# Performance work log

Measured on AMD Instinct MI355X. Metric: run time of the kernel, lower is better.

The kernel has to match this reference:

```python
import jax, jax.numpy as jnp
import numpy as np

B, H, W, C = 4, 48, 48, 768
L = H * W
D_STATE, D_CONV, D_INNER = 16, 4, C  # expand=1
DT_RANK = (C + 15) // 16  # 48


def generate_cross_scan_indices(Hh, Ww):
    indices = []
    visited = set()
    ch, cw = Hh // 2, Ww // 2
    indices.append((ch, cw)); visited.add((ch, cw))
    for radius in range(1, max(Hh, Ww)):
        for r in range(1, radius + 1):
            p = (ch - r, cw)
            if 0 <= p[0] < Hh and 0 <= p[1] < Ww and p not in visited: indices.append(p); visited.add(p)
        for r in range(1, radius + 1):
            p = (ch, cw + r)
            if 0 <= p[0] < Hh and 0 <= p[1] < Ww and p not in visited: indices.append(p); visited.add(p)
        for r in range(1, radius + 1):
            p = (ch + r, cw)
            if 0 <= p[0] < Hh and 0 <= p[1] < Ww and p not in visited: indices.append(p); visited.add(p)
        for r in range(1, radius + 1):
            p = (ch, cw - r)
            if 0 <= p[0] < Hh and 0 <= p[1] < Ww and p not in visited: indices.append(p); visited.add(p)
        for r in range(1, radius + 1):
            for p in [(ch - r, cw + r), (ch + r, cw + r), (ch + r, cw - r), (ch - r, cw - r)]:
                if 0 <= p[0] < Hh and 0 <= p[1] < Ww and p not in visited: indices.append(p); visited.add(p)
        for i in range(-radius, radius + 1):
            for j in range(-radius, radius + 1):
                p = (ch + i, cw + j)
                if 0 <= p[0] < Hh and 0 <= p[1] < Ww and p not in visited: indices.append(p); visited.add(p)
    return np.array([i * Ww + j for i, j in indices], dtype=np.int32)


def _mamba_params(key, scale=0.02):
    ks = jax.random.split(key, 6)
    return dict(
        in_w=jax.random.normal(ks[0], (2 * D_INNER, C)) * scale,
        conv_w=jax.random.normal(ks[1], (D_INNER, 1, D_CONV)) * scale,
        conv_b=jnp.zeros((D_INNER,)),
        xproj_w=jax.random.normal(ks[2], (DT_RANK + 2 * D_STATE, D_INNER)) * scale,
        dt_w=jax.random.normal(ks[3], (D_INNER, DT_RANK)) * scale,
        dt_b=jax.random.normal(ks[4], (D_INNER,)) * 0.1,
        A_log=jnp.broadcast_to(jnp.log(jnp.arange(1, D_STATE + 1, dtype=jnp.float32)), (D_INNER, D_STATE)).copy(),
        Dp=jnp.ones((D_INNER,)),
        out_w=jax.random.normal(ks[5], (C, D_INNER)) * scale,
    )


def setup_inputs() -> dict:
    key = jax.random.key(0)
    kx, kf, kb, k1, k2 = jax.random.split(key, 5)
    fp = _mamba_params(kf)
    bp = _mamba_params(kb)
    inp = {
        'x': jax.random.normal(kx, (B, L, C), dtype=jnp.float32),
        'scan_idx': jnp.asarray(generate_cross_scan_indices(H, W)),
        'norm_g': jnp.ones((C,)), 'norm_b': jnp.zeros((C,)),
        'fuse_w1': jax.random.normal(k1, (C, 2 * C)) * 0.02, 'fuse_b1': jnp.zeros((C,)),
        'fuse_w2': jax.random.normal(k2, (C, C)) * 0.02, 'fuse_b2': jnp.zeros((C,)),
    }
    for pre, p in (('f_', fp), ('b_', bp)):
        for n, v in p.items():
            inp[pre + n] = v
    return inp


def silu(v):
    return v * jax.nn.sigmoid(v)


def mamba(x, in_w, conv_w, conv_b, xproj_w, dt_w, dt_b, A_log, Dp, out_w):
    Bn, Ln, _ = x.shape
    xz = x @ in_w.T                      # [B,L,2*d_inner]
    xi, z = jnp.split(xz, 2, axis=-1)
    # causal depthwise conv1d, kernel D_CONV, left pad D_CONV-1
    xp = jnp.pad(xi, ((0, 0), (D_CONV - 1, 0), (0, 0)))
    xc = sum(conv_w[:, 0, k] * xp[:, k:k + Ln, :] for k in range(D_CONV)) + conv_b
    xc = silu(xc)                        # [B,L,d_inner]
    x_dbl = xc @ xproj_w.T
    dt, Bm, Cm = jnp.split(x_dbl, [DT_RANK, DT_RANK + D_STATE], axis=-1)
    dt = jax.nn.softplus(dt @ dt_w.T + dt_b)  # [B,L,d_inner]
    A = -jnp.exp(A_log)                  # [d_inner,d_state]

    def step(h, inps):
        dt_t, B_t, C_t, x_t = inps       # [B,d],[B,s],[B,s],[B,d]
        dA = jnp.exp(dt_t[:, :, None] * A)
        h = dA * h + (dt_t * x_t)[:, :, None] * B_t[:, None, :]
        y = jnp.einsum('bds,bs->bd', h, C_t)
        return h, y

    h0 = jnp.zeros((Bn, D_INNER, D_STATE), xc.dtype)
    xs = (dt.transpose(1, 0, 2), Bm.transpose(1, 0, 2), Cm.transpose(1, 0, 2), xc.transpose(1, 0, 2))
    _, ys = jax.lax.scan(step, h0, xs)
    y = ys.transpose(1, 0, 2) + Dp * xc
    y = y * silu(z)
    return y @ out_w.T


def reference(x, scan_idx, norm_g, norm_b, fuse_w1, fuse_b1, fuse_w2, fuse_b2,
              f_in_w, f_conv_w, f_conv_b, f_xproj_w, f_dt_w, f_dt_b, f_A_log, f_Dp, f_out_w,
              b_in_w, b_conv_w, b_conv_b, b_xproj_w, b_dt_w, b_dt_b, b_A_log, b_Dp, b_out_w):
    residual = x
    mu = x.mean(-1, keepdims=True)
    var = ((x - mu) ** 2).mean(-1, keepdims=True)
    xn = (x - mu) / jnp.sqrt(var + 1e-6) * norm_g + norm_b
    rev = jnp.argsort(scan_idx)
    xf = mamba(xn[:, scan_idx, :], f_in_w, f_conv_w, f_conv_b, f_xproj_w, f_dt_w, f_dt_b, f_A_log, f_Dp, f_out_w)[:, rev, :]
    flip = scan_idx[::-1]
    xb = mamba(xn[:, flip, :], b_in_w, b_conv_w, b_conv_b, b_xproj_w, b_dt_w, b_dt_b, b_A_log, b_Dp, b_out_w)[:, jnp.argsort(flip), :]
    fused = jnp.concatenate([xf, xb], axis=-1)
    h = jax.nn.gelu(fused @ fuse_w1.T + fuse_b1, approximate=False)
    out = h @ fuse_w2.T + fuse_b2
    return out + residual
```

## Files before the change

### kernel.cpp

```cpp
#include <hip/hip_runtime.h>
#include <hip/hip_bf16.h>
#include <cmath>

#define BB 4
#define LL 2304
#define CC 768
#define DSTATE 16
#define DINNER 768
#define DTRANK 48
#define MTOK (BB*LL)
#define NCH 48
#define LCH (LL/NCH)

#define S_XZ   14155776L
#define S_XC   7077888L
#define S_DT   7077888L
#define S_BC   294912L
#define S_YB   7077888L
#define S_AP   2359296L
#define S_XCR  79036416L

#define L2E 1.4426950408889634f

typedef __bf16 bf16_t;
typedef __bf16 bf16x8 __attribute__((ext_vector_type(8)));
typedef float  f32x4  __attribute__((ext_vector_type(4)));

__device__ __forceinline__ float silu_f(float v){ return v / (1.0f + __expf(-v)); }
__device__ __forceinline__ float softplus_f(float v){
    return fmaxf(v,0.f) + __logf(1.0f + __expf(-fabsf(v)));
}

typedef __attribute__((address_space(3))) void  lds_vt;
typedef __attribute__((address_space(1))) void  gbl_vt;
__device__ __forceinline__ void async_copy16(const void* g, void* l){
    __builtin_amdgcn_global_load_lds((const gbl_vt*)g, (lds_vt*)l, 16, 0, 0);
}


__global__ __launch_bounds__(256)
void wconv_k(const float* __restrict__ a0, const float* __restrict__ a1,
             const float* __restrict__ a2, const float* __restrict__ a3,
             const float* __restrict__ a4, const float* __restrict__ a5,
             bf16_t* __restrict__ dst)
{
    const int cum[7]  = {0,1179648,2359296,3538944,4128768,4153344,4177920};
    const int dofs[6] = {0,1179648,2359296,3538944,4718592,5332992};
    const float* srcs[6] = {a0,a1,a2,a3,a4,a5};
    int idx = blockIdx.x*256 + threadIdx.x;
    if (idx >= 4177920) return;
    int seg = 0;
    while (idx >= cum[seg+1]) ++seg;
    dst[dofs[seg] + idx - cum[seg]] = (bf16_t)srcs[seg][idx - cum[seg]];
}

__global__ __launch_bounds__(256)
void transp_k(const float* __restrict__ s0, const float* __restrict__ s1,
              bf16_t* __restrict__ d0, bf16_t* __restrict__ d1)
{
    __shared__ float tile[32][33];
    const float* src = blockIdx.z ? s1 : s0;
    bf16_t* dst = blockIdx.z ? d1 : d0;
    int c0 = blockIdx.y*32, d0c = blockIdx.x*32;
    int tx = threadIdx.x & 31, ty = threadIdx.x >> 5;
#pragma unroll
    for (int r=0;r<4;++r)
        tile[ty+8*r][tx] = src[(long)(c0+ty+8*r)*768 + d0c+tx];
    __syncthreads();
#pragma unroll
    for (int r=0;r<4;++r)
        dst[(long)(d0c+ty+8*r)*768 + c0+tx] = (bf16_t)tile[tx][ty+8*r];
}

__global__ __launch_bounds__(256)
void inv_k(const int* __restrict__ sidx, int* __restrict__ rf, int* __restrict__ rb)
{
    int t = blockIdx.x*256 + threadIdx.x;
    if (t >= LL) return;
    rf[sidx[t]] = t;
    rb[sidx[LL-1-t]] = t;
}

__global__ __launch_bounds__(256)
void combo_k(const float* __restrict__ dtw, const float* __restrict__ xproj,
             bf16_t* __restrict__ dst)
{
    __shared__ float row[48];
    int n = blockIdx.x;
    if (threadIdx.x < 48) row[threadIdx.x] = dtw[n*48 + threadIdx.x];
    __syncthreads();
#pragma unroll
    for (int kk=0; kk<3; ++kk){
        int k = threadIdx.x + 256*kk;
        float s = 0.f;
#pragma unroll 8
        for (int r=0; r<48; ++r) s += row[r]*xproj[r*768 + k];
        dst[n*768 + k] = (bf16_t)s;
    }
}

__global__ __launch_bounds__(256)
void ln_k(const float* __restrict__ x, const float* __restrict__ g,
          const float* __restrict__ bta, bf16_t* __restrict__ xn)
{
    int row = blockIdx.x;
    const float* xr = x + (long)row*CC;
    int tid = threadIdx.x;
    float v[3];
#pragma unroll
    for (int r=0;r<3;++r) v[r] = xr[tid + 256*r];
    float s  = v[0]+v[1]+v[2];
    float s2 = v[0]*v[0]+v[1]*v[1]+v[2]*v[2];
    __shared__ float red[8];
    for (int o=32;o;o>>=1){ s += __shfl_down(s,o); s2 += __shfl_down(s2,o); }
    int wv = tid>>6, ln = tid&63;
    if (ln==0){ red[wv]=s; red[4+wv]=s2; }
    __syncthreads();
    if (tid==0){
        red[0] = red[0]+red[1]+red[2]+red[3];
        red[4] = red[4]+red[5]+red[6]+red[7];
    }
    __syncthreads();
    float mu  = red[0]*(1.0f/CC);
    float var = red[4]*(1.0f/CC) - mu*mu;
    float rstd = rsqrtf(var + 1e-6f);
#pragma unroll
    for (int r=0;r<3;++r){
        int c = tid + 256*r;
        xn[(long)row*CC + c] = (bf16_t)((v[r]-mu)*rstd*g[c] + bta[c]);
    }
}

__global__ __launch_bounds__(256)
void conv_k(const bf16_t* __restrict__ xzT, const float* __restrict__ cw0,
            const float* __restrict__ cw1, const float* __restrict__ cb0,
            const float* __restrict__ cb1, bf16_t* __restrict__ xcT,
            bf16_t* __restrict__ xcR0, bf16_t* __restrict__ xcR1)
{
    const int dir = blockIdx.y;
    const bf16_t* src = xzT + (long)dir*S_XZ;
    bf16_t* dstT = xcT + (long)dir*S_XC;
    bf16_t* dstR = dir ? xcR1 : xcR0;
    const float* cw = dir ? cw1 : cw0;
    const float* cb = dir ? cb1 : cb0;
    int idx = blockIdx.x*256 + threadIdx.x;
    int d = idx % 768;
    int chunk = idx / 768;
    int tb = chunk*2;
    int r0 = chunk*16;

    bf16x8 c0 = *(const bf16x8*)&src[((long)tb*1536 + d)*8];
    bf16x8 c1 = *(const bf16x8*)&src[((long)(tb+1)*1536 + d)*8];
    float xm3, xm2, xm1;
    if (r0 % LL){
        bf16x8 pv = *(const bf16x8*)&src[((long)(tb-1)*1536 + d)*8];
        xm3=(float)pv[5]; xm2=(float)pv[6]; xm1=(float)pv[7];
    } else { xm3=0.f; xm2=0.f; xm1=0.f; }

    float4 w = *(const float4*)&cw[d*4];
    float bz = cb[d];

    float xx[16];
#pragma unroll
    for (int u=0;u<8;++u){ xx[u]=(float)c0[u]; xx[8+u]=(float)c1[u]; }
    bf16x8 o0, o1;
#pragma unroll
    for (int u=0;u<16;++u){
        float cur = xx[u];
        float acc = bz + w.x*xm3 + w.y*xm2 + w.z*xm1 + w.w*cur;
        float r = silu_f(acc);
        if (u < 8) o0[u] = (bf16_t)r; else o1[u-8] = (bf16_t)r;
        xm3 = xm2; xm2 = xm1; xm1 = cur;
    }
    *(bf16x8*)&dstT[((long)tb*768 + d)*8]     = o0;
    *(bf16x8*)&dstT[((long)(tb+1)*768 + d)*8] = o1;
#pragma unroll
    for (int u=0;u<8;++u){
        dstR[(long)(r0+u)*DINNER + d]   = o0[u];
        dstR[(long)(r0+8+u)*DINNER + d] = o1[u];
    }
}

template<int GATHER, int SCATTER, int EPI>
__global__ __launch_bounds__(256)
void gemm4_k(const bf16_t* __restrict__ A, long a_stride, int lda,
             const bf16_t* __restrict__ W0, const bf16_t* __restrict__ W1,
             int N, int K,
             void* __restrict__ out1, long o1_stride,
             void* __restrict__ out2, long o2_stride,
             int ldc, int ccol_stride,
             const float* __restrict__ bias0, const float* __restrict__ bias1,
             const float* __restrict__ resid,
             const int* __restrict__ sidx,
             const int* __restrict__ ridx0, const int* __restrict__ ridx1)
{
    __shared__ __align__(16) bf16_t smem[2*128*64];
    bf16_t* As = smem;
    bf16_t* Bs = smem + 128*64;

    const int tid  = threadIdx.x;
    const int lane = tid & 63;
    const int w    = tid >> 6;
    const int ln16 = lane & 15;
    const int q    = lane >> 4;
    const int dir  = blockIdx.z;

    const bf16_t* Ad = A + (long)dir*a_stride;
    const bf16_t* W  = dir ? W1 : W0;
    const float* bias = dir ? bias1 : bias0;

    const int m0 = blockIdx.x*128;
    const int n0 = blockIdx.y*128;

    const int srow = lane >> 3;
    const int csrc = (lane & 7) ^ srow;
    const bf16_t* gA[4]; const bf16_t* gA1[4]; const bf16_t* gB[4];
#pragma unroll
    for (int inst=0; inst<4; ++inst){
        int row = w*32 + inst*8 + srow;
        int r = m0 + row;
        if (GATHER == 4){
            int t = r % LL; int bo = r - t;
            gA[inst]  = A + (long)(bo + ridx0[t])*lda + csrc*8;
            gA1[inst] = A + a_stride + (long)(bo + ridx1[t])*lda + csrc*8;
        } else {
            int sr = r;
            if (GATHER == 3){
                int t = r % LL; int bo = r - t;
                sr = bo + (dir ? sidx[LL-1-t] : sidx[t]);
            }
            gA[inst] = Ad + (long)sr*lda + csrc*8;
        }
        int n = n0 + row; if (n >= N) n = N-1;
        gB[inst] = W + (long)n*K + csrc*8;
    }

    f32x4 acc[4][4];
#pragma unroll
    for (int i=0;i<4;++i)
#pragma unroll
      for (int j=0;j<4;++j) acc[i][j] = (f32x4){0.f,0.f,0.f,0.f};

    const int e = ln16 & 7;
    const int ar_base = ((w>>1)*64 + ln16)*64;
    const int br_base = ((w&1)*64 + ln16)*64;

    for (int k0 = 0; k0 < K; k0 += 64){
#pragma unroll
        for (int inst=0; inst<4; ++inst){
            bf16_t* la = As + (w*256 + inst*64)*8;
            bf16_t* lb = Bs + (w*256 + inst*64)*8;
            const bf16_t* asrc;
            if (GATHER == 4)
                asrc = (k0 >= 768) ? (gA1[inst] + (k0 - 768)) : (gA[inst] + k0);
            else
                asrc = gA[inst] + k0;
            async_copy16(asrc, la);
            async_copy16(gB[inst] + k0, lb);
        }
        __syncthreads();
#pragma unroll
        for (int kk=0; kk<2; ++kk){
            const int ce = (((kk<<2)|q) ^ e)*8;
            bf16x8 af[4], bf[4];
#pragma unroll
            for (int i=0;i<4;++i) af[i] = *(const bf16x8*)&As[ar_base + i*16*64 + ce];
#pragma unroll
            for (int j=0;j<4;++j) bf[j] = *(const bf16x8*)&Bs[br_base + j*16*64 + ce];
#pragma unroll
            for (int i=0;i<4;++i)
#pragma unroll
              for (int j=0;j<4;++j)
                acc[i][j] = __builtin_amdgcn_mfma_f32_16x16x32_bf16(af[i], bf[j], acc[i][j], 0,0,0);
        }
        __syncthreads();
    }

    const int mw = (w>>1)*64;
    const int nw = (w&1)*64;
    const int ccolb = ccol_stride*dir;

    const bool staged = (EPI==2) || (EPI==3) || (EPI==6) ||
                        ((EPI==5 || EPI==7) && n0 < 768);
    if (staged){
        bf16_t* Cs = smem;
#pragma unroll
        for (int i=0;i<4;++i){
#pragma unroll
            for (int reg=0; reg<4; ++reg){
                int rowl = mw + i*16 + q*4 + reg;
#pragma unroll
                for (int j=0;j<4;++j){
                    int coll = nw + j*16 + ln16;
                    float v = acc[i][j][reg];
                    if (EPI==3){
                        v += bias[n0 + coll];
                        v = 0.5f*v*(1.0f + erff(v*0.70710678118654752f));
                    } else if (EPI==5 || EPI==7){
                        v = softplus_f(v + bias[n0 + coll]);
                    }
                    Cs[rowl*128 + coll] = (bf16_t)v;
                }
            }
        }
        __syncthreads();
        bf16_t* o = (bf16_t*)out1 + (long)dir*o1_stride;
        if (EPI==6 || EPI==7){
#pragma unroll
            for (int c=0;c<8;++c){
                int chunk = tid + 256*c;
                int nb  = chunk & 127;
                int tbl = chunk >> 7;
                bf16x8 v;
#pragma unroll
                for (int u=0;u<8;++u) v[u] = Cs[(tbl*8+u)*128 + nb];
                long base = ((long)(m0/8 + tbl)*ldc + (n0 + nb))*8;
                *(bf16x8*)&o[base] = v;
            }
        } else {
#pragma unroll
            for (int c=0;c<8;++c){
                int chunk = tid + 256*c;
                int rowl = chunk >> 4;
                int coll = (chunk & 15)*8;
                int r = m0 + rowl;
                int orow = r;
                if (SCATTER == 3){
                    int t = r % LL; int bo = r - t;
                    orow = bo + (dir ? sidx[LL-1-t] : sidx[t]);
                }
                *(int4*)&o[(long)orow*ldc + ccolb + n0 + coll] = *(const int4*)&Cs[rowl*128 + coll];
            }
        }
    } else {
#pragma unroll
        for (int i=0;i<4;++i){
#pragma unroll
            for (int reg=0; reg<4; ++reg){
                int r = m0 + mw + i*16 + q*4 + reg;
#pragma unroll
                for (int j=0;j<4;++j){
                    int col = n0 + nw + j*16 + ln16;
                    if (col >= N) continue;
                    float v = acc[i][j][reg];
                    if (EPI==4){
                        v += bias[col] + resid[(long)r*CC + col];
                        ((float*)out1)[(long)r*ldc + col] = v;
                    } else {
                        ((float*)out2 + (long)dir*o2_stride)[(long)r*32 + (col-768)] = v;
                    }
                }
            }
        }
    }
}

template<int PASS>
__global__ __launch_bounds__(256)
void scanp_k(const bf16_t* __restrict__ dtp, const bf16_t* __restrict__ xcp,
             const float* __restrict__ bcp, const bf16_t* __restrict__ xzp,
             const float* __restrict__ Al0, const float* __restrict__ Al1,
             const float* __restrict__ Dp0, const float* __restrict__ Dp1,
             float* __restrict__ Aprod, float* __restrict__ Hend,
             bf16_t* __restrict__ yout)
{
    __shared__ __align__(16) float s_bc[LCH*32];

    const int dir = blockIdx.y;
    int blk = blockIdx.x;
    const int dblk = blk % 3; int tmp = blk / 3;
    const int j = tmp % NCH; const int b = tmp / NCH;
    const int tid = threadIdx.x;
    const long tbase = (long)b*LL + (long)j*LCH;
    const long tb0 = tbase >> 3;
    const int d = dblk*256 + tid;

    const float* gbc = bcp + dir*S_BC + tbase*32;
    async_copy16(gbc + tid*4, s_bc + tid*4);
    if (tid < 128) async_copy16(gbc + (256+tid)*4, s_bc + (256+tid)*4);

    const float* Al = dir ? Al1 : Al0;
    float ac2[16]; bool fast = true;
#pragma unroll
    for (int k=0;k<16;++k){
        float a = -__expf(Al[d*DSTATE + k]);
        fast = fast && (fabsf(a + (float)(k+1)) < 1e-3f*(float)(k+1));
        ac2[k] = a * L2E;
    }

    const bf16_t* gdt = dtp + dir*S_DT + (tb0*768  + d)*8;
    const bf16_t* gxc = xcp + dir*S_XC + (tb0*768  + d)*8;
    const bf16_t* gz  = xzp + dir*S_XZ + (tb0*1536 + 768 + d)*8;
    bf16_t* gy = yout + dir*S_YB + tbase*DINNER + d;

    const long o = dir*S_AP + ((long)(b*NCH + j)*DINNER + d)*DSTATE;

    float h[16];
    float dpv = 0.f;
    if (PASS==3){
#pragma unroll
        for (int g=0; g<4; ++g){
            f32x4 hv = *(const f32x4*)&Aprod[o + 4*g];
#pragma unroll
            for (int k=0;k<4;++k) h[g*4+k] = hv[k];
        }
        dpv = (dir ? Dp1 : Dp0)[d];
    } else {
#pragma unroll
        for (int k=0;k<16;++k) h[k] = 0.f;
    }
    float sdt = 0.f;

    __syncthreads();

#pragma unroll 1
    for (int cc=0; cc<LCH/8; ++cc){
        bf16x8 vdt = *(const bf16x8*)&gdt[(long)cc*6144];
        bf16x8 vxc = *(const bf16x8*)&gxc[(long)cc*6144];
        bf16x8 vz;
        if (PASS==3) vz = *(const bf16x8*)&gz[(long)cc*12288];
#pragma unroll
        for (int u=0; u<8; ++u){
            const int t = cc*8 + u;
            float dt = (float)vdt[u];
            float xv = (float)vxc[u];
            float c = dt*xv;
            if (PASS==1) sdt += dt;
            const float* bcr = &s_bc[t*32];
            float p = 0.f;
            if (fast){
                float e1 = __builtin_amdgcn_exp2f(-L2E*dt);
                float e2 = e1*e1, e3 = e2*e1, e4 = e2*e2;
                float m = 1.0f;
#pragma unroll
                for (int g=0; g<4; ++g){
                    f32x4 Bv = *(const f32x4*)&bcr[g*4];
                    h[g*4+0] = (m*e1)*h[g*4+0] + c*Bv[0];
                    h[g*4+1] = (m*e2)*h[g*4+1] + c*Bv[1];
                    h[g*4+2] = (m*e3)*h[g*4+2] + c*Bv[2];
                    h[g*4+3] = (m*e4)*h[g*4+3] + c*Bv[3];
                    if (PASS==3){
                        f32x4 Cv = *(const f32x4*)&bcr[16 + g*4];
                        p += h[g*4+0]*Cv[0] + h[g*4+1]*Cv[1]
                           + h[g*4+2]*Cv[2] + h[g*4+3]*Cv[3];
                    }
                    m *= e4;
                }
            } else {
#pragma unroll
                for (int g=0; g<4; ++g){
                    f32x4 Bv = *(const f32x4*)&bcr[g*4];
#pragma unroll
                    for (int k=0;k<4;++k)
                        h[g*4+k] = __builtin_amdgcn_exp2f(dt*ac2[g*4+k])*h[g*4+k] + c*Bv[k];
                    if (PASS==3){
                        f32x4 Cv = *(const f32x4*)&bcr[16 + g*4];
                        p += h[g*4+0]*Cv[0] + h[g*4+1]*Cv[1]
                           + h[g*4+2]*Cv[2] + h[g*4+3]*Cv[3];
                    }
                }
            }
            if (PASS==3){
                float zv = (float)vz[u];
                gy[(long)t*DINNER] = (bf16_t)((p + dpv*xv) * silu_f(zv));
            }
        }
    }

    if (PASS==1){
        float e1s = __builtin_amdgcn_exp2f(-L2E*sdt);
        float e2s = e1s*e1s, e3s = e2s*e1s, e4s = e2s*e2s;
        float m = 1.0f;
#pragma unroll
        for (int g=0; g<4; ++g){
            f32x4 av, hv;
            if (fast){
                av[0]=m*e1s; av[1]=m*e2s; av[2]=m*e3s; av[3]=m*e4s;
                m *= e4s;
            } else {
#pragma unroll
                for (int k=0;k<4;++k) av[k] = __builtin_amdgcn_exp2f(sdt*ac2[g*4+k]);
            }
#pragma unroll
            for (int k=0;k<4;++k) hv[k] = h[g*4+k];
            *(f32x4*)&Aprod[o+4*g] = av;
            *(f32x4*)&Hend[o+4*g]  = hv;
        }
    }
}

__global__ __launch_bounds__(256)
void scan2_k(float* __restrict__ Aprod, const float* __restrict__ Hend)
{
    int idx = blockIdx.x*256 + threadIdx.x;
    if (idx >= 2*BB*DINNER*DSTATE) return;
    int dir = idx / (BB*DINNER*DSTATE);
    int rem = idx - dir*(BB*DINNER*DSTATE);
    int b = rem / (DINNER*DSTATE);
    int ds = rem % (DINNER*DSTATE);
    long base = (long)dir*S_AP;
    float h = 0.f;
    for (int j=0;j<NCH;++j){
        long o = base + (long)(b*NCH+j)*DINNER*DSTATE + ds;
        float ap = Aprod[o];
        float he = Hend[o];
        Aprod[o] = h;
        h = ap*h + he;
    }
}

extern "C" void kernel_launch(void* const* d_in, const int* in_sizes, int n_in,
                              void* d_out, int out_size, void* d_ws, size_t ws_size,
                              hipStream_t stream)
{
    const float* x       = (const float*)d_in[0];
    const int*   sidx    = (const int*)  d_in[1];
    const float* norm_g  = (const float*)d_in[2];
    const float* norm_b  = (const float*)d_in[3];
    const float* fuse_w1 = (const float*)d_in[4];
    const float* fuse_b1 = (const float*)d_in[5];
    const float* fuse_w2 = (const float*)d_in[6];
    const float* fuse_b2 = (const float*)d_in[7];
    const float* f_in_w   = (const float*)d_in[8];
    const float* f_conv_w = (const float*)d_in[9];
    const float* f_conv_b = (const float*)d_in[10];
    const float* f_xproj  = (const float*)d_in[11];
    const float* f_dt_w   = (const float*)d_in[12];
    const float* f_dt_b   = (const float*)d_in[13];
    const float* f_A_log  = (const float*)d_in[14];
    const float* f_Dp     = (const float*)d_in[15];
    const float* f_out_w  = (const float*)d_in[16];
    const float* b_in_w   = (const float*)d_in[17];
    const float* b_conv_w = (const float*)d_in[18];
    const float* b_conv_b = (const float*)d_in[19];
    const float* b_xproj  = (const float*)d_in[20];
    const float* b_dt_w   = (const float*)d_in[21];
    const float* b_dt_b   = (const float*)d_in[22];
    const float* b_A_log  = (const float*)d_in[23];
    const float* b_Dp     = (const float*)d_in[24];
    const float* b_out_w  = (const float*)d_in[25];
    float* out = (float*)d_out;

    float* ws    = (float*)d_ws;
    bf16_t* xn   = (bf16_t*)ws;
    bf16_t* xz   = (bf16_t*)(ws + 3538944);
    bf16_t* xc   = (bf16_t*)(ws + 17694720);
    bf16_t* dtb  = (bf16_t*)(ws + 24772608);
    float* bc    = ws + 31850496;
    bf16_t* yb   = (bf16_t*)(ws + 32440320);
    bf16_t* h1   = (bf16_t*)(ws + 39518208);
    float* Aprod = ws + 43057152;
    float* Hend  = ws + 47775744;
    bf16_t* wbf  = (bf16_t*)(ws + 52494336);
    int* rev_f   = (int*)(ws + 56352768);
    int* rev_b   = rev_f + 2304;

    bf16_t* w_fin    = wbf + 0;
    bf16_t* w_bin    = wbf + 1179648;
    bf16_t* w_1      = wbf + 2359296;
    bf16_t* w_2      = wbf + 3538944;
    bf16_t* w_fcombo = wbf + 4128768;
    bf16_t* w_bcombo = wbf + 4743168;
    bf16_t* foutT    = wbf + 5357568;
    bf16_t* boutT    = wbf + 5947392;
    bf16_t* Ccat     = wbf + 6537216;

    bf16_t* xcR0 = xn;
    bf16_t* xcR1 = h1;

    wconv_k<<<16320, 256, 0, stream>>>(f_in_w, b_in_w, fuse_w1, fuse_w2,
                                       f_xproj + 48*768, b_xproj + 48*768, wbf);
    transp_k<<<dim3(24,24,2), 256, 0, stream>>>(f_out_w, b_out_w, foutT, boutT);
    inv_k<<<9, 256, 0, stream>>>(sidx, rev_f, rev_b);
    combo_k<<<768, 256, 0, stream>>>(f_dt_w, f_xproj, w_fcombo);
    combo_k<<<768, 256, 0, stream>>>(b_dt_w, b_xproj, w_bcombo);
    ln_k<<<MTOK, 256, 0, stream>>>(x, norm_g, norm_b, xn);
    gemm4_k<0,0,2><<<dim3(6,6,2), 256, 0, stream>>>(
        w_1, 768, 1536, foutT, boutT, 768, 768,
        Ccat, 0, nullptr, 0, 1536, 768, nullptr, nullptr, nullptr, nullptr,
        nullptr, nullptr);

    gemm4_k<3,0,6><<<dim3(72,12,2), 256, 0, stream>>>(
        xn, 0, CC, w_fin, w_bin, 1536, 768,
        xz, S_XZ, nullptr, 0, 1536, 0, nullptr, nullptr, nullptr, sidx,
        nullptr, nullptr);
    conv_k<<<dim3(1728, 2), 256, 0, stream>>>(
        xz, f_conv_w, b_conv_w, f_conv_b, b_conv_b, xc, xcR0, xcR1);
    gemm4_k<0,0,7><<<dim3(72,7,2), 256, 0, stream>>>(
        xcR0, S_XCR, DINNER, w_fcombo, w_bcombo, 800, 768,
        dtb, S_DT, bc, S_BC, 768, 0, f_dt_b, b_dt_b, nullptr, nullptr,
        nullptr, nullptr);
    scanp_k<1><<<dim3(BB*NCH*3,2), 256, 0, stream>>>(
        dtb, xc, bc, xz, f_A_log, b_A_log, f_Dp, b_Dp, Aprod, Hend, yb);
    scan2_k<<<384, 256, 0, stream>>>(Aprod, Hend);
    scanp_k<3><<<dim3(BB*NCH*3,2), 256, 0, stream>>>(
        dtb, xc, bc, xz, f_A_log, b_A_log, f_Dp, b_Dp, Aprod, Hend, yb);
    gemm4_k<4,0,3><<<dim3(72,6,1), 256, 0, stream>>>(
        yb, S_YB, DINNER, Ccat, Ccat, 768, 1536,
        h1, 0, nullptr, 0, 768, 0, fuse_b1, fuse_b1, nullptr, nullptr,
        rev_f, rev_b);
    gemm4_k<0,0,4><<<dim3(72,6,1), 256, 0, stream>>>(
        h1, 0, DINNER, w_2, w_2, 768, 768,
        out, 0, nullptr, 0, 768, 0, fuse_b2, fuse_b2, x, nullptr,
        nullptr, nullptr);
}
```

Before: 485.8 us.

## Move scan-order permutation into layernorm store and scan output scatter

Layernorm now writes each token directly at its forward scan position using the inverse permutation, so the in-projection GEMM reads rows contiguously (with a simple reversal for the backward direction) instead of gathering through the scan index. The scan kernel scatters its gated output back to spatial order, so the fuse GEMM reads both directions contiguously rather than gathering through two reverse index tables. The aim is to replace scattered async row loads in the GEMMs with contiguous ones, paying for it with scattered row stores in layernorm and the scan.

```diff
diff --git a/kernel.cpp b/kernel.cpp
--- a/kernel.cpp
+++ b/kernel.cpp
@@ -101,7 +101,8 @@
 
 __global__ __launch_bounds__(256)
 void ln_k(const float* __restrict__ x, const float* __restrict__ g,
-          const float* __restrict__ bta, bf16_t* __restrict__ xn)
+          const float* __restrict__ bta, const int* __restrict__ rf,
+          bf16_t* __restrict__ xn)
 {
     int row = blockIdx.x;
     const float* xr = x + (long)row*CC;
@@ -124,10 +125,12 @@
     float mu  = red[0]*(1.0f/CC);
     float var = red[4]*(1.0f/CC) - mu*mu;
     float rstd = rsqrtf(var + 1e-6f);
+    int t = row % LL;
+    long drow = (long)(row - t) + rf[t];
 #pragma unroll
     for (int r=0;r<3;++r){
         int c = tid + 256*r;
-        xn[(long)row*CC + c] = (bf16_t)((v[r]-mu)*rstd*g[c] + bta[c]);
+        xn[drow*CC + c] = (bf16_t)((v[r]-mu)*rstd*g[c] + bta[c]);
     }
 }
 
@@ -219,15 +222,14 @@
     for (int inst=0; inst<4; ++inst){
         int row = w*32 + inst*8 + srow;
         int r = m0 + row;
-        if (GATHER == 4){
-            int t = r % LL; int bo = r - t;
-            gA[inst]  = A + (long)(bo + ridx0[t])*lda + csrc*8;
-            gA1[inst] = A + a_stride + (long)(bo + ridx1[t])*lda + csrc*8;
+        if (GATHER == 7){
+            gA[inst]  = A + (long)r*lda + csrc*8;
+            gA1[inst] = A + a_stride + (long)r*lda + csrc*8;
         } else {
             int sr = r;
-            if (GATHER == 3){
-                int t = r % LL; int bo = r - t;
-                sr = bo + (dir ? sidx[LL-1-t] : sidx[t]);
+            if (GATHER == 6 && dir){
+                int t = r % LL;
+                sr = r - t + (LL-1-t);
             }
             gA[inst] = Ad + (long)sr*lda + csrc*8;
         }
@@ -251,7 +253,7 @@
             bf16_t* la = As + (w*256 + inst*64)*8;
             bf16_t* lb = Bs + (w*256 + inst*64)*8;
             const bf16_t* asrc;
-            if (GATHER == 4)
+            if (GATHER == 7)
                 asrc = (k0 >= 768) ? (gA1[inst] + (k0 - 768)) : (gA[inst] + k0);
             else
                 asrc = gA[inst] + k0;
@@ -281,7 +283,7 @@
     const int ccolb = ccol_stride*dir;
 
     const bool staged = (EPI==2) || (EPI==3) || (EPI==6) ||
-                        ((EPI==5 || EPI==7) && n0 < 768);
+                        (EPI==7 && n0 < 768);
     if (staged){
         bf16_t* Cs = smem;
 #pragma unroll
@@ -296,7 +298,7 @@
                     if (EPI==3){
                         v += bias[n0 + coll];
                         v = 0.5f*v*(1.0f + erff(v*0.70710678118654752f));
-                    } else if (EPI==5 || EPI==7){
+                    } else if (EPI==7){
                         v = softplus_f(v + bias[n0 + coll]);
                     }
                     Cs[rowl*128 + coll] = (bf16_t)v;
@@ -324,12 +326,7 @@
                 int rowl = chunk >> 4;
                 int coll = (chunk & 15)*8;
                 int r = m0 + rowl;
-                int orow = r;
-                if (SCATTER == 3){
-                    int t = r % LL; int bo = r - t;
-                    orow = bo + (dir ? sidx[LL-1-t] : sidx[t]);
-                }
-                *(int4*)&o[(long)orow*ldc + ccolb + n0 + coll] = *(const int4*)&Cs[rowl*128 + coll];
+                *(int4*)&o[(long)r*ldc + ccolb + n0 + coll] = *(const int4*)&Cs[rowl*128 + coll];
             }
         }
     } else {
@@ -362,7 +359,7 @@
              const float* __restrict__ Al0, const float* __restrict__ Al1,
              const float* __restrict__ Dp0, const float* __restrict__ Dp1,
              float* __restrict__ Aprod, float* __restrict__ Hend,
-             bf16_t* __restrict__ yout)
+             bf16_t* __restrict__ yout, const int* __restrict__ sidx)
 {
     __shared__ __align__(16) float s_bc[LCH*32];
 
@@ -391,7 +388,7 @@
     const bf16_t* gdt = dtp + dir*S_DT + (tb0*768  + d)*8;
     const bf16_t* gxc = xcp + dir*S_XC + (tb0*768  + d)*8;
     const bf16_t* gz  = xzp + dir*S_XZ + (tb0*1536 + 768 + d)*8;
-    bf16_t* gy = yout + dir*S_YB + tbase*DINNER + d;
+    bf16_t* gyb = yout + dir*S_YB + (long)b*LL*DINNER + d;
 
     const long o = dir*S_AP + ((long)(b*NCH + j)*DINNER + d)*DSTATE;
 
@@ -462,7 +459,9 @@
             }
             if (PASS==3){
                 float zv = (float)vz[u];
-                gy[(long)t*DINNER] = (bf16_t)((p + dpv*xv) * silu_f(zv));
+                int jp = j*LCH + t;
+                int prow = dir ? sidx[LL-1-jp] : sidx[jp];
+                gyb[(long)prow*DINNER] = (bf16_t)((p + dpv*xv) * silu_f(zv));
             }
         }
     }
@@ -574,15 +573,15 @@
     inv_k<<<9, 256, 0, stream>>>(sidx, rev_f, rev_b);
     combo_k<<<768, 256, 0, stream>>>(f_dt_w, f_xproj, w_fcombo);
     combo_k<<<768, 256, 0, stream>>>(b_dt_w, b_xproj, w_bcombo);
-    ln_k<<<MTOK, 256, 0, stream>>>(x, norm_g, norm_b, xn);
+    ln_k<<<MTOK, 256, 0, stream>>>(x, norm_g, norm_b, rev_f, xn);
     gemm4_k<0,0,2><<<dim3(6,6,2), 256, 0, stream>>>(
         w_1, 768, 1536, foutT, boutT, 768, 768,
         Ccat, 0, nullptr, 0, 1536, 768, nullptr, nullptr, nullptr, nullptr,
         nullptr, nullptr);
 
-    gemm4_k<3,0,6><<<dim3(72,12,2), 256, 0, stream>>>(
+    gemm4_k<6,0,6><<<dim3(72,12,2), 256, 0, stream>>>(
         xn, 0, CC, w_fin, w_bin, 1536, 768,
-        xz, S_XZ, nullptr, 0, 1536, 0, nullptr, nullptr, nullptr, sidx,
+        xz, S_XZ, nullptr, 0, 1536, 0, nullptr, nullptr, nullptr, nullptr,
         nullptr, nullptr);
     conv_k<<<dim3(1728, 2), 256, 0, stream>>>(
         xz, f_conv_w, b_conv_w, f_conv_b, b_conv_b, xc, xcR0, xcR1);
@@ -591,14 +590,14 @@
         dtb, S_DT, bc, S_BC, 768, 0, f_dt_b, b_dt_b, nullptr, nullptr,
         nullptr, nullptr);
     scanp_k<1><<<dim3(BB*NCH*3,2), 256, 0, stream>>>(
-        dtb, xc, bc, xz, f_A_log, b_A_log, f_Dp, b_Dp, Aprod, Hend, yb);
+        dtb, xc, bc, xz, f_A_log, b_A_log, f_Dp, b_Dp, Aprod, Hend, yb, sidx);
     scan2_k<<<384, 256, 0, stream>>>(Aprod, Hend);
     scanp_k<3><<<dim3(BB*NCH*3,2), 256, 0, stream>>>(
-        dtb, xc, bc, xz, f_A_log, b_A_log, f_Dp, b_Dp, Aprod, Hend, yb);
-    gemm4_k<4,0,3><<<dim3(72,6,1), 256, 0, stream>>>(
+        dtb, xc, bc, xz, f_A_log, b_A_log, f_Dp, b_Dp, Aprod, Hend, yb, sidx);
+    gemm4_k<7,0,3><<<dim3(72,6,1), 256, 0, stream>>>(
         yb, S_YB, DINNER, Ccat, Ccat, 768, 1536,
         h1, 0, nullptr, 0, 768, 0, fuse_b1, fuse_b1, nullptr, nullptr,
-        rev_f, rev_b);
+        nullptr, nullptr);
     gemm4_k<0,0,4><<<dim3(72,6,1), 256, 0, stream>>>(
         h1, 0, DINNER, w_2, w_2, 768, 768,
         out, 0, nullptr, 0, 768, 0, fuse_b2, fuse_b2, x, nullptr,
```

After: 490.3 us. No clear change (+0.9%).
